# Kernel optimization log

Hardware: AMD Instinct MI355X
Metric: run time of the kernel (lower is better)

Reference implementation:

```python
import jax, jax.numpy as jnp
import numpy as np
from jax import lax

TOP_K = 4
N_GROUP = 4
TOPK_GROUP = 2
ROUTED_SCALING = 2.5
NORM_TOPK = True


def relu2(v):
    r = jax.nn.relu(v)
    return r * r


def setup_inputs() -> dict:
    key = jax.random.key(0)
    ks = jax.random.split(key, 7)
    B, S, H, E, I, IS = 2, 2048, 1024, 16, 512, 2048
    x = jax.random.normal(ks[0], (B, S, H), dtype=jnp.float32)
    router_w = jax.random.normal(ks[1], (E, H), dtype=jnp.float32) * 0.02
    bias = jnp.zeros((E,), dtype=jnp.float32)
    w_up = jax.random.normal(ks[2], (E, I, H), dtype=jnp.float32) * 0.02
    w_down = jax.random.normal(ks[3], (E, H, I), dtype=jnp.float32) * 0.02
    ws_up = jax.random.normal(ks[4], (IS, H), dtype=jnp.float32) * 0.02
    ws_down = jax.random.normal(ks[5], (H, IS), dtype=jnp.float32) * 0.02
    return {"x": x, "router_w": router_w, "bias": bias, "w_up": w_up,
            "w_down": w_down, "ws_up": ws_up, "ws_down": ws_down,
            "attn_metadata": 0}


def _route(xf, router_w, bias):
    # xf: [T, H] float32
    T = xf.shape[0]
    E = router_w.shape[0]
    logits = xf @ router_w.T                      # [T, E]
    scores = jax.nn.sigmoid(logits)
    sfc = scores + bias[None, :]                  # scores_for_choice
    # group scores: sum of top-2 within each group
    g = sfc.reshape(T, N_GROUP, E // N_GROUP)
    group_scores = lax.top_k(g, 2)[0].sum(-1)     # [T, G]
    _, gidx = lax.top_k(group_scores, TOPK_GROUP)
    gmask = jax.nn.one_hot(gidx, N_GROUP, dtype=sfc.dtype).sum(1)  # [T, G]
    smask = jnp.repeat(gmask, E // N_GROUP, axis=1)                # [T, E]
    masked = jnp.where(smask > 0, sfc, 0.0)
    _, tidx = lax.top_k(masked, TOP_K)            # [T, K]
    tw = jnp.take_along_axis(scores, tidx, axis=1)
    if NORM_TOPK:
        tw = tw / (tw.sum(-1, keepdims=True) + 1e-20)
    tw = tw * ROUTED_SCALING
    return tidx, tw


def reference(x, router_w, bias, w_up, w_down, ws_up, ws_down, attn_metadata):
    B, S, H = x.shape
    E = w_up.shape[0]
    xf = x.reshape(-1, H).astype(jnp.float32)     # [T, H]
    tidx, tw = _route(xf, router_w, bias)
    # combine weights per (token, expert): scatter-add topk weights
    T = xf.shape[0]
    comb = jnp.zeros((T, E), dtype=tw.dtype).at[jnp.arange(T)[:, None], tidx].add(tw)
    # routed experts (dense grouped form; zero combine weight == not routed)
    up = jnp.einsum('th,eih->tei', xf, w_up)      # [T, E, I]
    h = relu2(up) * comb[:, :, None]
    routed = jnp.einsum('tei,ehi->th', h, w_down) # [T, H]
    routed = routed.reshape(B, S, H).astype(x.dtype)
    # shared expert on residual
    shared = relu2(jnp.einsum('bsh,ih->bsi', x, ws_up))
    shared = jnp.einsum('bsi,hi->bsh', shared, ws_down)
    return routed + shared
```

## Files before the change

kernel.cpp:

```cpp
#include <hip/hip_runtime.h>
#include <stdint.h>

#define T_TOK 4096
#define H_DIM 1024
#define E_NUM 16
#define I_DIM 512
#define IS_DIM 2048
#define TOPK 4
#define NGRP 4
#define GSZ 4
#define MAXMT 32
#define NCHUNK 64

#define W0 524288
#define W1 1048576
#define W2 3145728
#define W3 5242880
#define CVT_NB 2048

typedef unsigned short u16;
typedef __attribute__((ext_vector_type(8))) short short8;
typedef __attribute__((ext_vector_type(4))) float f32x4;

__device__ __forceinline__ void gload16(const void* g, void* l) {
  __builtin_amdgcn_global_load_lds(
      (const __attribute__((address_space(1))) void*)g,
      (__attribute__((address_space(3))) void*)l, 16, 0, 0);
}

__device__ __forceinline__ u16 f2bf(float f) {
  union { float f; uint32_t u; } v; v.f = f;
  uint32_t u = v.u;
  uint32_t r = (u + 0x7fffu + ((u >> 16) & 1u)) >> 16;
  return (u16)r;
}

__device__ __forceinline__ float bf2f(u16 h) {
  union { uint32_t u; float f; } v; v.u = ((uint32_t)h) << 16;
  return v.f;
}

__global__ __launch_bounds__(256) void cvt_w_kernel(
    const float* __restrict__ wsu, const float* __restrict__ wsd,
    const float* __restrict__ wu, const float* __restrict__ wd,
    u16* __restrict__ wsub, u16* __restrict__ wsdb,
    u16* __restrict__ wub, u16* __restrict__ wdb) {
  for (int i = blockIdx.x * 256 + threadIdx.x; i < W3; i += CVT_NB * 256) {
    const float4* src; ushort4* dst; int base;
    if (i < W0)      { src = (const float4*)wsu; dst = (ushort4*)wsub; base = 0;  }
    else if (i < W1) { src = (const float4*)wsd; dst = (ushort4*)wsdb; base = W0; }
    else if (i < W2) { src = (const float4*)wu;  dst = (ushort4*)wub;  base = W1; }
    else             { src = (const float4*)wd;  dst = (ushort4*)wdb;  base = W2; }
    float4 v = src[i - base];
    ushort4 o;
    o.x = f2bf(v.x); o.y = f2bf(v.y); o.z = f2bf(v.z); o.w = f2bf(v.w);
    dst[i - base] = o;
  }
}

__global__ __launch_bounds__(256) void route_kernel(
    const float* __restrict__ x, const float* __restrict__ rw,
    const float* __restrict__ bias, int* __restrict__ tidx_out,
    float* __restrict__ tw_out, u16* __restrict__ x_bf) {
  const int wave = threadIdx.x >> 6;
  const int lane = threadIdx.x & 63;
  const int t = blockIdx.x * 4 + wave;

  const float4* xr = reinterpret_cast<const float4*>(x + (size_t)t * H_DIM);
  const float4* rw4 = reinterpret_cast<const float4*>(rw);
  ushort4* xbw = reinterpret_cast<ushort4*>(x_bf + (size_t)t * H_DIM);
  float4 xv[4];
#pragma unroll
  for (int j = 0; j < 4; ++j) xv[j] = xr[lane + j * 64];
#pragma unroll
  for (int j = 0; j < 4; ++j) {
    ushort4 o;
    o.x = f2bf(xv[j].x); o.y = f2bf(xv[j].y);
    o.z = f2bf(xv[j].z); o.w = f2bf(xv[j].w);
    xbw[lane + j * 64] = o;
  }

  double acc[E_NUM];
#pragma unroll
  for (int e = 0; e < E_NUM; ++e) {
    double a = 0.0;
#pragma unroll
    for (int j = 0; j < 4; ++j) {
      float4 w = rw4[e * 256 + lane + j * 64];
      a += (double)xv[j].x * (double)w.x;
      a += (double)xv[j].y * (double)w.y;
      a += (double)xv[j].z * (double)w.z;
      a += (double)xv[j].w * (double)w.w;
    }
    acc[e] = a;
  }
#pragma unroll
  for (int e = 0; e < E_NUM; ++e) {
#pragma unroll
    for (int off = 32; off; off >>= 1) acc[e] += __shfl_xor(acc[e], off);
  }
  if (lane == 0) {
    float scores[E_NUM], sfc[E_NUM];
#pragma unroll
    for (int e = 0; e < E_NUM; ++e) {
      scores[e] = 1.0f / (1.0f + expf((float)(-acc[e])));
      sfc[e] = scores[e] + bias[e];
    }
    float gs[NGRP];
#pragma unroll
    for (int g = 0; g < NGRP; ++g) {
      float m1 = -1e30f, m2 = -1e30f;
#pragma unroll
      for (int j = 0; j < GSZ; ++j) {
        float v = sfc[g * GSZ + j];
        if (v > m1) { m2 = m1; m1 = v; } else if (v > m2) { m2 = v; }
      }
      gs[g] = m1 + m2;
    }
    int g1 = 0;
    for (int g = 1; g < NGRP; ++g) if (gs[g] > gs[g1]) g1 = g;
    int g2 = -1;
    for (int g = 0; g < NGRP; ++g) {
      if (g == g1) continue;
      if (g2 < 0 || gs[g] > gs[g2]) g2 = g;
    }
    float masked[E_NUM];
#pragma unroll
    for (int e = 0; e < E_NUM; ++e) {
      int g = e / GSZ;
      masked[e] = (g == g1 || g == g2) ? sfc[e] : 0.0f;
    }
    int tidx[TOPK]; float tw[TOPK];
#pragma unroll
    for (int k = 0; k < TOPK; ++k) {
      int best = 0; float bv = masked[0];
      for (int e = 1; e < E_NUM; ++e)
        if (masked[e] > bv) { bv = masked[e]; best = e; }
      tidx[k] = best; tw[k] = scores[best]; masked[best] = -1e30f;
    }
    float s = tw[0] + tw[1] + tw[2] + tw[3] + 1e-20f;
#pragma unroll
    for (int k = 0; k < TOPK; ++k) {
      tidx_out[t * TOPK + k] = tidx[k];
      tw_out[t * TOPK + k] = tw[k] / s * 2.5f;
    }
  }
}

__global__ __launch_bounds__(256) void hist_kernel(const int* __restrict__ tidx,
                                                   int* __restrict__ partial) {
  const int c = blockIdx.x;
  const int tid = threadIdx.x;
  const int lane = tid & 63;
  const int w = tid >> 6;
  __shared__ int h[4][E_NUM];
  const int e = tidx[c * 256 + tid];
#pragma unroll
  for (int ee = 0; ee < E_NUM; ++ee) {
    unsigned long long b = __ballot(e == ee);
    if (lane == 0) h[w][ee] = __popcll(b);
  }
  __syncthreads();
  if (tid < E_NUM)
    partial[c * E_NUM + tid] = h[0][tid] + h[1][tid] + h[2][tid] + h[3][tid];
}

__global__ __launch_bounds__(256) void prefix2_kernel(
    const int* __restrict__ partial, int* __restrict__ chunk_base,
    int* __restrict__ counts, int* __restrict__ offsets) {
  __shared__ int tot[E_NUM];
  __shared__ int offs[E_NUM];
  const int tid = threadIdx.x;
  if (tid < E_NUM) {
    int run = 0;
    for (int c = 0; c < NCHUNK; ++c) {
      chunk_base[c * E_NUM + tid] = run;
      run += partial[c * E_NUM + tid];
    }
    tot[tid] = run;
    counts[tid] = run;
  }
  __syncthreads();
  if (tid == 0) {
    int s = 0;
    for (int e = 0; e < E_NUM; ++e) { offs[e] = s; offsets[e] = s; s += tot[e]; }
    offsets[E_NUM] = s;
  }
  __syncthreads();
  for (int i = tid; i < NCHUNK * E_NUM; i += 256)
    chunk_base[i] += offs[i & 15];
}

__global__ __launch_bounds__(256) void scatter2_kernel(
    const int* __restrict__ tidx, const float* __restrict__ tw,
    const int* __restrict__ chunk_base,
    int* __restrict__ tok_g, float* __restrict__ w_g, int* __restrict__ pos_map) {
  const int c = blockIdx.x;
  const int tid = threadIdx.x;
  const int lane = tid & 63;
  const int w = tid >> 6;
  __shared__ int h[4][E_NUM];
  const int i = c * 256 + tid;
  const int e = tidx[i];
  int pre = 0;
#pragma unroll
  for (int ee = 0; ee < E_NUM; ++ee) {
    unsigned long long b = __ballot(e == ee);
    if (lane == 0) h[w][ee] = __popcll(b);
    if (ee == e) pre = __popcll(b & ((1ull << lane) - 1ull));
  }
  __syncthreads();
  int rank = pre;
  for (int ww = 0; ww < w; ++ww) rank += h[ww][e];
  const int pos = chunk_base[c * E_NUM + e] + rank;
  tok_g[pos] = i >> 2;
  w_g[pos] = tw[i];
  pos_map[i] = pos;
}

#define NB_UP 5120
__global__ __launch_bounds__(256, 3) void gemm_up(
    const u16* __restrict__ x_bf, const u16* __restrict__ wsup_bf,
    const u16* __restrict__ wup_bf, u16* __restrict__ hs, u16* __restrict__ hp,
    const int* __restrict__ counts, const int* __restrict__ offsets,
    const int* __restrict__ tok_g, const float* __restrict__ w_g) {
  __shared__ __align__(16) u16 As[2][128 * 64];
  __shared__ __align__(16) u16 Bs[2][64 * 64];

  const int cpx = gridDim.x >> 3;
  const int wg = (blockIdx.x & 7) * cpx + (blockIdx.x >> 3);
  const int q = wg / 5;
  const int r5 = wg - q * 5;
  const bool shared = (r5 == 0);

  int mt, nt, cnt, obase = 0;
  const u16* B;
  if (shared) {
    mt = q >> 5;
    nt = q & 31;
    cnt = T_TOK;
    B = wsup_bf;
  } else {
    int rid = q * 4 + (r5 - 1);
    int e = rid >> 8;
    int r = rid & 255;
    mt = r >> 3;
    nt = r & 7;
    cnt = counts[e];
    if (mt * 128 >= cnt) return;
    obase = offsets[e];
    B = wup_bf + (size_t)e * (I_DIM * H_DIM);
  }
  const int K = H_DIM;

  const int tid = threadIdx.x;
  const int srow = tid >> 3;
  const int slot = tid & 7;
  const u16* gA[4];
#pragma unroll
  for (int p = 0; p < 4; ++p) {
    int rloc = p * 32 + srow;
    int ks = ((slot ^ (rloc & 7)) << 3);
    int am = mt * 128 + rloc;
    int row;
    if (shared) row = am;
    else row = tok_g[obase + ((am < cnt) ? am : 0)];
    gA[p] = x_bf + (size_t)row * H_DIM + ks;
  }
  const u16* gB[2];
#pragma unroll
  for (int p = 0; p < 2; ++p) {
    int rloc = p * 32 + srow;
    int ks = ((slot ^ (rloc & 7)) << 3);
    gB[p] = B + (size_t)(nt * 64 + rloc) * K + ks;
  }

  const int wave = tid >> 6;
  const int lane = tid & 63;
  const int wr = wave >> 1;
  const int wc = wave & 1;
  const int frow = lane & 15;
  const int l4 = lane >> 4;

  int a_off[4][2], b_off[2][2];
#pragma unroll
  for (int m = 0; m < 4; ++m) {
    int row = wr * 64 + m * 16 + frow;
#pragma unroll
    for (int kk = 0; kk < 2; ++kk)
      a_off[m][kk] = (row << 6) + ((((kk << 2) + l4) ^ (row & 7)) << 3);
  }
#pragma unroll
  for (int n = 0; n < 2; ++n) {
    int row = wc * 32 + n * 16 + frow;
#pragma unroll
    for (int kk = 0; kk < 2; ++kk)
      b_off[n][kk] = (row << 6) + ((((kk << 2) + l4) ^ (row & 7)) << 3);
  }

  f32x4 acc[4][2];
#pragma unroll
  for (int m = 0; m < 4; ++m)
#pragma unroll
    for (int n = 0; n < 2; ++n) acc[m][n] = (f32x4)0.0f;

  const int dst = tid << 3;
  auto stage = [&](int k0, int c) {
#pragma unroll
    for (int p = 0; p < 4; ++p)
      gload16(gA[p] + k0, &As[c][(p << 11) + dst]);
#pragma unroll
    for (int p = 0; p < 2; ++p)
      gload16(gB[p] + k0, &Bs[c][(p << 11) + dst]);
  };

  const int KT = K >> 6;
  stage(0, 0);
  int cur = 0;
  for (int kt = 0; kt < KT; ++kt) {
    __syncthreads();
    if (kt + 1 < KT) stage((kt + 1) << 6, cur ^ 1);
#pragma unroll
    for (int kk = 0; kk < 2; ++kk) {
      short8 a[4], b[2];
#pragma unroll
      for (int m = 0; m < 4; ++m)
        a[m] = *reinterpret_cast<const short8*>(&As[cur][a_off[m][kk]]);
#pragma unroll
      for (int n = 0; n < 2; ++n)
        b[n] = *reinterpret_cast<const short8*>(&Bs[cur][b_off[n][kk]]);
      __builtin_amdgcn_s_setprio(1);
#pragma unroll
      for (int m = 0; m < 4; ++m)
#pragma unroll
        for (int n = 0; n < 2; ++n)
          acc[m][n] = __builtin_amdgcn_mfma_f32_16x16x32_bf16(a[m], b[n], acc[m][n], 0, 0, 0);
      __builtin_amdgcn_s_setprio(0);
    }
    cur ^= 1;
  }

  const int rbase = l4 << 2;
  const int cbase = frow;
#pragma unroll
  for (int m = 0; m < 4; ++m) {
#pragma unroll
    for (int r = 0; r < 4; ++r) {
      int lr = wr * 64 + (m << 4) + rbase + r;
      int grow = mt * 128 + lr;
      if (!shared && grow >= cnt) continue;
      float wv = shared ? 1.0f : w_g[obase + grow];
#pragma unroll
      for (int n = 0; n < 2; ++n) {
        int gc = nt * 64 + wc * 32 + (n << 4) + cbase;
        float v = acc[m][n][r];
        float tpos = fmaxf(v, 0.0f);
        float o = tpos * tpos * wv;
        if (shared) hs[(size_t)grow * IS_DIM + gc] = f2bf(o);
        else hp[(size_t)(obase + grow) * I_DIM + gc] = f2bf(o);
      }
    }
  }
}

template <int EPI>
__global__ __launch_bounds__(256, 3) void gemm_bt(
    const u16* __restrict__ Abase, const u16* __restrict__ Bbase,
    float* __restrict__ Cf, u16* __restrict__ Cb,
    int M, int N, int K,
    const int* __restrict__ counts, const int* __restrict__ offsets,
    const int* __restrict__ tok_g, const float* __restrict__ w_g,
    const int* __restrict__ pos_map, const u16* __restrict__ Rd) {
  __shared__ __align__(16) u16 As[2][128 * 64];
  __shared__ __align__(16) u16 Bs[2][64 * 64];

  const int cpx = gridDim.x >> 3;
  const int wg = (blockIdx.x & 7) * cpx + (blockIdx.x >> 3);

  const int NT = N >> 6;
  int mt, nt, cnt = M, obase = 0;
  const u16* A = Abase;
  const u16* B = Bbase;

  if constexpr (EPI == 1) {
    mt = wg / NT;
    nt = wg - mt * NT;
  } else {
    const int per_e = MAXMT * NT;
    int e = wg / per_e;
    int r = wg - e * per_e;
    mt = r / NT;
    nt = r - mt * NT;
    cnt = counts[e];
    if (mt * 128 >= cnt) return;
    obase = offsets[e];
    A = Abase + (size_t)obase * I_DIM;
    B = Bbase + (size_t)e * (H_DIM * I_DIM);
  }

  const int tid = threadIdx.x;
  const int srow = tid >> 3;
  const int slot = tid & 7;
  const u16* gA[4];
#pragma unroll
  for (int p = 0; p < 4; ++p) {
    int rloc = p * 32 + srow;
    int ks = ((slot ^ (rloc & 7)) << 3);
    int am = mt * 128 + rloc;
    if constexpr (EPI == 3) {
      gA[p] = A + (size_t)((am < cnt) ? am : 0) * K + ks;
    } else {
      gA[p] = A + (size_t)am * K + ks;
    }
  }
  const u16* gB[2];
#pragma unroll
  for (int p = 0; p < 2; ++p) {
    int rloc = p * 32 + srow;
    int ks = ((slot ^ (rloc & 7)) << 3);
    gB[p] = B + (size_t)(nt * 64 + rloc) * K + ks;
  }

  const int wave = tid >> 6;
  const int lane = tid & 63;
  const int wr = wave >> 1;
  const int wc = wave & 1;
  const int frow = lane & 15;
  const int l4 = lane >> 4;

  int a_off[4][2], b_off[2][2];
#pragma unroll
  for (int m = 0; m < 4; ++m) {
    int row = wr * 64 + m * 16 + frow;
#pragma unroll
    for (int kk = 0; kk < 2; ++kk)
      a_off[m][kk] = (row << 6) + ((((kk << 2) + l4) ^ (row & 7)) << 3);
  }
#pragma unroll
  for (int n = 0; n < 2; ++n) {
    int row = wc * 32 + n * 16 + frow;
#pragma unroll
    for (int kk = 0; kk < 2; ++kk)
      b_off[n][kk] = (row << 6) + ((((kk << 2) + l4) ^ (row & 7)) << 3);
  }

  f32x4 acc[4][2];
#pragma unroll
  for (int m = 0; m < 4; ++m)
#pragma unroll
    for (int n = 0; n < 2; ++n) acc[m][n] = (f32x4)0.0f;

  const int dst = tid << 3;
  auto stage = [&](int k0, int c) {
#pragma unroll
    for (int p = 0; p < 4; ++p)
      gload16(gA[p] + k0, &As[c][(p << 11) + dst]);
#pragma unroll
    for (int p = 0; p < 2; ++p)
      gload16(gB[p] + k0, &Bs[c][(p << 11) + dst]);
  };

  const int KT = K >> 6;
  stage(0, 0);
  int cur = 0;
  for (int kt = 0; kt < KT; ++kt) {
    __syncthreads();
    if (kt + 1 < KT) stage((kt + 1) << 6, cur ^ 1);
#pragma unroll
    for (int kk = 0; kk < 2; ++kk) {
      short8 a[4], b[2];
#pragma unroll
      for (int m = 0; m < 4; ++m)
        a[m] = *reinterpret_cast<const short8*>(&As[cur][a_off[m][kk]]);
#pragma unroll
      for (int n = 0; n < 2; ++n)
        b[n] = *reinterpret_cast<const short8*>(&Bs[cur][b_off[n][kk]]);
      __builtin_amdgcn_s_setprio(1);
#pragma unroll
      for (int m = 0; m < 4; ++m)
#pragma unroll
        for (int n = 0; n < 2; ++n)
          acc[m][n] = __builtin_amdgcn_mfma_f32_16x16x32_bf16(a[m], b[n], acc[m][n], 0, 0, 0);
      __builtin_amdgcn_s_setprio(0);
    }
    cur ^= 1;
  }

  const int rbase = l4 << 2;
  const int cbase = frow;
#pragma unroll
  for (int m = 0; m < 4; ++m) {
#pragma unroll
    for (int r = 0; r < 4; ++r) {
      int lr = wr * 64 + (m << 4) + rbase + r;
      int grow = mt * 128 + lr;
      if (EPI == 3 && grow >= cnt) continue;
      const int* pm = nullptr;
      if constexpr (EPI == 1) pm = pos_map + grow * TOPK;
#pragma unroll
      for (int n = 0; n < 2; ++n) {
        int gc = nt * 64 + wc * 32 + (n << 4) + cbase;
        float v = acc[m][n][r];
        if constexpr (EPI == 1) {
          v += bf2f(Rd[(size_t)pm[0] * H_DIM + gc]);
          v += bf2f(Rd[(size_t)pm[1] * H_DIM + gc]);
          v += bf2f(Rd[(size_t)pm[2] * H_DIM + gc]);
          v += bf2f(Rd[(size_t)pm[3] * H_DIM + gc]);
          Cf[(size_t)grow * N + gc] = v;
        } else {
          Cb[(size_t)(obase + grow) * N + gc] = f2bf(v);
        }
      }
    }
  }
}

extern "C" void kernel_launch(void* const* d_in, const int* in_sizes, int n_in,
                              void* d_out, int out_size, void* d_ws, size_t ws_size,
                              hipStream_t stream) {
  const float* x = (const float*)d_in[0];
  const float* rw = (const float*)d_in[1];
  const float* bias = (const float*)d_in[2];
  const float* w_up = (const float*)d_in[3];
  const float* w_down = (const float*)d_in[4];
  const float* ws_up = (const float*)d_in[5];
  const float* ws_down = (const float*)d_in[6];
  float* out = (float*)d_out;

  uint8_t* wsb = (uint8_t*)d_ws;
  size_t off = 0;
  auto alloc = [&](size_t bytes) {
    void* p = wsb + off;
    off += (bytes + 255) & ~(size_t)255;
    return p;
  };
  u16* x_bf = (u16*)alloc((size_t)T_TOK * H_DIM * 2);
  u16* wsup_bf = (u16*)alloc((size_t)IS_DIM * H_DIM * 2);
  u16* wsdn_bf = (u16*)alloc((size_t)H_DIM * IS_DIM * 2);
  u16* wup_bf = (u16*)alloc((size_t)E_NUM * I_DIM * H_DIM * 2);
  u16* wdn_bf = (u16*)alloc((size_t)E_NUM * H_DIM * I_DIM * 2);
  u16* hs = (u16*)alloc((size_t)T_TOK * IS_DIM * 2);
  u16* hp = (u16*)alloc((size_t)(T_TOK * TOPK + 128) * I_DIM * 2);
  u16* hp_down = (u16*)alloc((size_t)(T_TOK * TOPK + 128) * H_DIM * 2);
  int* counts = (int*)alloc(64);
  int* offsets = (int*)alloc(128);
  int* tok_g = (int*)alloc((size_t)(T_TOK * TOPK) * 4);
  float* w_g = (float*)alloc((size_t)(T_TOK * TOPK) * 4);
  int* pos_map = (int*)alloc((size_t)(T_TOK * TOPK) * 4);
  int* tidx_buf = (int*)alloc((size_t)T_TOK * TOPK * 4);
  float* tw_buf = (float*)alloc((size_t)T_TOK * TOPK * 4);
  int* partial = (int*)alloc((size_t)NCHUNK * E_NUM * 4);
  int* chunk_base = (int*)alloc((size_t)NCHUNK * E_NUM * 4);

  route_kernel<<<T_TOK / 4, 256, 0, stream>>>(x, rw, bias, tidx_buf, tw_buf, x_bf);
  hist_kernel<<<NCHUNK, 256, 0, stream>>>(tidx_buf, partial);
  prefix2_kernel<<<1, 256, 0, stream>>>(partial, chunk_base, counts, offsets);
  scatter2_kernel<<<NCHUNK, 256, 0, stream>>>(tidx_buf, tw_buf, chunk_base,
                                              tok_g, w_g, pos_map);
  cvt_w_kernel<<<CVT_NB, 256, 0, stream>>>(
      ws_up, ws_down, w_up, w_down, wsup_bf, wsdn_bf, wup_bf, wdn_bf);

  gemm_up<<<NB_UP, 256, 0, stream>>>(
      x_bf, wsup_bf, wup_bf, hs, hp, counts, offsets, tok_g, w_g);
  gemm_bt<3><<<E_NUM * MAXMT * (H_DIM / 64), 256, 0, stream>>>(
      hp, wdn_bf, nullptr, hp_down, T_TOK, H_DIM, I_DIM,
      counts, offsets, tok_g, w_g, nullptr, nullptr);
  gemm_bt<1><<<(T_TOK / 128) * (H_DIM / 64), 256, 0, stream>>>(
      hs, wsdn_bf, out, nullptr, T_TOK, H_DIM, IS_DIM,
      nullptr, nullptr, nullptr, nullptr, pos_map, hp_down);
}
```

Baseline: 193.9 us.

## Triple-buffer LDS tiles with prefetch distance two in MoE GEMMs

Both GEMM kernels move from a double-buffered LDS pipeline to a three-stage ring, issuing global-to-LDS loads two K-tiles ahead. A partial vmcnt wait plus a raw s_barrier replaces __syncthreads, so the next tile's loads can stay in flight while the current tile is consumed. This is meant to hide more memory latency per block. In exchange LDS use grows to 72KB per block, so launch bounds drop from 3 to 2 blocks per CU, which reduces occupancy.

```diff
diff --git a/kernel.cpp b/kernel.cpp
--- a/kernel.cpp
+++ b/kernel.cpp
@@ -219,13 +219,13 @@
 }
 
 #define NB_UP 5120
-__global__ __launch_bounds__(256, 3) void gemm_up(
+__global__ __launch_bounds__(256, 2) void gemm_up(
     const u16* __restrict__ x_bf, const u16* __restrict__ wsup_bf,
     const u16* __restrict__ wup_bf, u16* __restrict__ hs, u16* __restrict__ hp,
     const int* __restrict__ counts, const int* __restrict__ offsets,
     const int* __restrict__ tok_g, const float* __restrict__ w_g) {
-  __shared__ __align__(16) u16 As[2][128 * 64];
-  __shared__ __align__(16) u16 Bs[2][64 * 64];
+  __shared__ __align__(16) u16 As[3][128 * 64];
+  __shared__ __align__(16) u16 Bs[3][64 * 64];
 
   const int cpx = gridDim.x >> 3;
   const int wg = (blockIdx.x & 7) * cpx + (blockIdx.x >> 3);
@@ -316,19 +316,26 @@
 
   const int KT = K >> 6;
   stage(0, 0);
-  int cur = 0;
+  stage(64, 1);
+  int cb = 0, sb = 2;
   for (int kt = 0; kt < KT; ++kt) {
-    __syncthreads();
-    if (kt + 1 < KT) stage((kt + 1) << 6, cur ^ 1);
+    if (kt < KT - 1) {
+      asm volatile("s_waitcnt vmcnt(6)" ::: "memory");
+    } else {
+      asm volatile("s_waitcnt vmcnt(0)" ::: "memory");
+    }
+    __builtin_amdgcn_s_barrier();
+    __builtin_amdgcn_sched_barrier(0);
+    if (kt + 2 < KT) stage((kt + 2) << 6, sb);
 #pragma unroll
     for (int kk = 0; kk < 2; ++kk) {
       short8 a[4], b[2];
 #pragma unroll
       for (int m = 0; m < 4; ++m)
-        a[m] = *reinterpret_cast<const short8*>(&As[cur][a_off[m][kk]]);
+        a[m] = *reinterpret_cast<const short8*>(&As[cb][a_off[m][kk]]);
 #pragma unroll
       for (int n = 0; n < 2; ++n)
-        b[n] = *reinterpret_cast<const short8*>(&Bs[cur][b_off[n][kk]]);
+        b[n] = *reinterpret_cast<const short8*>(&Bs[cb][b_off[n][kk]]);
       __builtin_amdgcn_s_setprio(1);
 #pragma unroll
       for (int m = 0; m < 4; ++m)
@@ -337,7 +344,8 @@
           acc[m][n] = __builtin_amdgcn_mfma_f32_16x16x32_bf16(a[m], b[n], acc[m][n], 0, 0, 0);
       __builtin_amdgcn_s_setprio(0);
     }
-    cur ^= 1;
+    cb = (cb == 2) ? 0 : cb + 1;
+    sb = (sb == 2) ? 0 : sb + 1;
   }
 
   const int rbase = l4 << 2;
@@ -364,15 +372,15 @@
 }
 
 template <int EPI>
-__global__ __launch_bounds__(256, 3) void gemm_bt(
+__global__ __launch_bounds__(256, 2) void gemm_bt(
     const u16* __restrict__ Abase, const u16* __restrict__ Bbase,
     float* __restrict__ Cf, u16* __restrict__ Cb,
     int M, int N, int K,
     const int* __restrict__ counts, const int* __restrict__ offsets,
     const int* __restrict__ tok_g, const float* __restrict__ w_g,
     const int* __restrict__ pos_map, const u16* __restrict__ Rd) {
-  __shared__ __align__(16) u16 As[2][128 * 64];
-  __shared__ __align__(16) u16 Bs[2][64 * 64];
+  __shared__ __align__(16) u16 As[3][128 * 64];
+  __shared__ __align__(16) u16 Bs[3][64 * 64];
 
   const int cpx = gridDim.x >> 3;
   const int wg = (blockIdx.x & 7) * cpx + (blockIdx.x >> 3);
@@ -462,19 +470,26 @@
 
   const int KT = K >> 6;
   stage(0, 0);
-  int cur = 0;
+  stage(64, 1);
+  int cb = 0, sb = 2;
   for (int kt = 0; kt < KT; ++kt) {
-    __syncthreads();
-    if (kt + 1 < KT) stage((kt + 1) << 6, cur ^ 1);
+    if (kt < KT - 1) {
+      asm volatile("s_waitcnt vmcnt(6)" ::: "memory");
+    } else {
+      asm volatile("s_waitcnt vmcnt(0)" ::: "memory");
+    }
+    __builtin_amdgcn_s_barrier();
+    __builtin_amdgcn_sched_barrier(0);
+    if (kt + 2 < KT) stage((kt + 2) << 6, sb);
 #pragma unroll
     for (int kk = 0; kk < 2; ++kk) {
       short8 a[4], b[2];
 #pragma unroll
       for (int m = 0; m < 4; ++m)
-        a[m] = *reinterpret_cast<const short8*>(&As[cur][a_off[m][kk]]);
+        a[m] = *reinterpret_cast<const short8*>(&As[cb][a_off[m][kk]]);
 #pragma unroll
       for (int n = 0; n < 2; ++n)
-        b[n] = *reinterpret_cast<const short8*>(&Bs[cur][b_off[n][kk]]);
+        b[n] = *reinterpret_cast<const short8*>(&Bs[cb][b_off[n][kk]]);
       __builtin_amdgcn_s_setprio(1);
 #pragma unroll
       for (int m = 0; m < 4; ++m)
@@ -483,7 +498,8 @@
           acc[m][n] = __builtin_amdgcn_mfma_f32_16x16x32_bf16(a[m], b[n], acc[m][n], 0, 0, 0);
       __builtin_amdgcn_s_setprio(0);
     }
-    cur ^= 1;
+    cb = (cb == 2) ? 0 : cb + 1;
+    sb = (sb == 2) ? 0 : sb + 1;
   }
 
   const int rbase = l4 << 2;
```

Result: slower. 223.3 us (+15.2%).
